# Kernel tuning notes

Measured on AMD Instinct MI355X. Metric: run time of the kernel, lower is better.

The kernel has to match this reference:

```python
import jax, jax.numpy as jnp
import numpy as np

B, T, M, D, H, DH = 2, 2048, 2048, 384, 4, 96
NM, DF, R, NA = 8, 1536, 16, 4
S = 0.02  # weight init scale

PARAM_NAMES = ['cWq','cbq','cWk','cbk','cWv','cbv','cWo','cbo',
               'sWq','sbq','sWk','sbk','sWv','sbv','sWo','sbo',
               'gW','gb','f1W','f1b','f2W','f2b','adA','adB',
               'ln1g','ln1b','ln2g','ln2b','ln3g','ln3b']

def setup_inputs() -> dict:
    key = jax.random.key(0)
    ks = jax.random.split(key, 20)
    n = lambda k, sh, s=1.0: jax.random.normal(k, sh, dtype=jnp.float32) * s
    z = lambda sh: jnp.zeros(sh, dtype=jnp.float32)
    o = lambda sh: jnp.ones(sh, dtype=jnp.float32)
    return {
        'x': n(ks[0], (B, T, D)),
        'mem': n(ks[1], (B, M, D)),
        'motif_ctrl': n(ks[2], (B, NM)),
        'adapter_idx': 1,
        'cWq': n(ks[3], (D, D), S), 'cbq': z((D,)),
        'cWk': n(ks[4], (D, D), S), 'cbk': z((D,)),
        'cWv': n(ks[5], (D, D), S), 'cbv': z((D,)),
        'cWo': n(ks[6], (D, D), S), 'cbo': z((D,)),
        'sWq': n(ks[7], (D, D), S), 'sbq': z((D,)),
        'sWk': n(ks[8], (D, D), S), 'sbk': z((D,)),
        'sWv': n(ks[9], (D, D), S), 'sbv': z((D,)),
        'sWo': n(ks[10], (D, D), S), 'sbo': z((D,)),
        'gW': n(ks[11], (H, NM), S), 'gb': z((H,)),
        'f1W': n(ks[12], (DF, D), S), 'f1b': z((DF,)),
        'f2W': n(ks[13], (D, DF), S), 'f2b': z((D,)),
        'adA': n(ks[14], (NA, R, D), S),
        'adB': n(ks[15], (NA, D, R), S),
        'ln1g': o((D,)), 'ln1b': z((D,)),
        'ln2g': o((D,)), 'ln2b': z((D,)),
        'ln3g': o((D,)), 'ln3b': z((D,)),
    }

def _lin(x, W, b):
    return x @ W.T + b  # torch nn.Linear convention: W is [out, in]

def _layernorm(x, g, b):
    mu = x.mean(-1, keepdims=True)
    var = ((x - mu) ** 2).mean(-1, keepdims=True)
    return (x - mu) * jax.lax.rsqrt(var + 1e-5) * g + b

def _block(x, mem, motif_ctrl, adapter_idx, p):
    scale = 1.0 / np.sqrt(DH).astype(np.float32)
    # --- cross-attention over memory ---
    h = _layernorm(x, p['ln1g'], p['ln1b'])
    q = _lin(h, p['cWq'], p['cbq']).reshape(B, T, H, DH)
    k = _lin(mem, p['cWk'], p['cbk']).reshape(B, M, H, DH)
    v = _lin(mem, p['cWv'], p['cbv']).reshape(B, M, H, DH)
    A = jax.nn.softmax(jnp.einsum('bthd,bmhd->bhtm', q, k) * scale, axis=-1)
    z = jnp.einsum('bhtm,bmhd->bthd', A, v).reshape(B, T, D)
    x = x + _lin(z, p['cWo'], p['cbo'])
    # --- motif-gated self-attention (post-softmax per-head gate) ---
    h = _layernorm(x, p['ln2g'], p['ln2b'])
    gates = jax.nn.sigmoid(motif_ctrl @ p['gW'].T + p['gb'])  # [B, H]
    q = _lin(h, p['sWq'], p['sbq']).reshape(B, T, H, DH)
    k = _lin(h, p['sWk'], p['sbk']).reshape(B, T, H, DH)
    v = _lin(h, p['sWv'], p['sbv']).reshape(B, T, H, DH)
    A = jax.nn.softmax(jnp.einsum('bthd,bshd->bhts', q, k) * scale, axis=-1)
    A = A * gates[:, :, None, None]
    z = jnp.einsum('bhts,bshd->bthd', A, v).reshape(B, T, D)
    x = x + _lin(z, p['sWo'], p['sbo'])
    # --- LoRA-adapter FFN ---
    h = _layernorm(x, p['ln3g'], p['ln3b'])
    f = _lin(jax.nn.gelu(_lin(h, p['f1W'], p['f1b']), approximate=False), p['f2W'], p['f2b'])
    f = f + (h @ p['adA'][adapter_idx].T) @ p['adB'][adapter_idx].T
    return x + f

def reference(x, mem, motif_ctrl, adapter_idx,
              cWq, cbq, cWk, cbk, cWv, cbv, cWo, cbo,
              sWq, sbq, sWk, sbk, sWv, sbv, sWo, sbo,
              gW, gb, f1W, f1b, f2W, f2b, adA, adB,
              ln1g, ln1b, ln2g, ln2b, ln3g, ln3b):
    p = dict(zip(PARAM_NAMES, (cWq, cbq, cWk, cbk, cWv, cbv, cWo, cbo,
                               sWq, sbq, sWk, sbk, sWv, sbv, sWo, sbo,
                               gW, gb, f1W, f1b, f2W, f2b, adA, adB,
                               ln1g, ln1b, ln2g, ln2b, ln3g, ln3b)))
    return _block(x, mem, motif_ctrl, int(adapter_idx), p)
```

## Files before the change

kernel.cpp:

```cpp
#include <hip/hip_runtime.h>
#include <hip/hip_bf16.h>
#include <math.h>

#define B_   2
#define T_   2048
#define M_   2048
#define D_   384
#define H_   4
#define DH_  96
#define NM_  8
#define DF_  1536
#define R_   16
#define NR_  4096

typedef unsigned short u16;
typedef u16    u16x8  __attribute__((ext_vector_type(8)));
typedef u16    u16x4  __attribute__((ext_vector_type(4)));
typedef __bf16 bf16x8 __attribute__((ext_vector_type(8)));
typedef float  f32x4  __attribute__((ext_vector_type(4)));

union V8 { u16x8 u; bf16x8 b; };
__device__ __forceinline__ bf16x8 as_bf(u16x8 x) { V8 v; v.u = x; return v.b; }

__device__ __forceinline__ u16 f2bf(float f) {
    unsigned u = __float_as_uint(f);
    unsigned r = (u + 0x7fffu + ((u >> 16) & 1u)) >> 16;
    return (u16)r;
}

__device__ __forceinline__ void load16(const u16* g, u16* l) {
    __builtin_amdgcn_global_load_lds(
        (const __attribute__((address_space(1))) void*)g,
        (__attribute__((address_space(3))) void*)l, 16, 0, 0);
}

__global__ __launch_bounds__(256)
void setup_kernel(const float* cWq, const float* cWk, const float* cWv, const float* cWo,
                  const float* sWq, const float* sWk, const float* sWv, const float* sWo,
                  const float* f1W, const float* f2W, const float* adA, const float* adB,
                  const float* mem,
                  u16* Wq_c, u16* Wkv_c, u16* Wco, u16* Wqkv_s, u16* Wso,
                  u16* Wf1, u16* Wf2, u16* WadA, u16* WadB, u16* memb,
                  const float* cbk, const float* cbv,
                  const float* sbq, const float* sbk, const float* sbv,
                  float* bkv_c, float* bqkv_s,
                  const float* mc, const float* gW, const float* gb, float* gates) {
    int seg = blockIdx.y;
    if (seg == 13) {
        for (int i = blockIdx.x * 256 + threadIdx.x; i < 1928; i += gridDim.x * 256) {
            if (i < 768) bkv_c[i] = (i < 384) ? cbk[i] : cbv[i - 384];
            else if (i < 1920) {
                int j = i - 768;
                bqkv_s[j] = (j < 384) ? sbq[j] : (j < 768 ? sbk[j - 384] : sbv[j - 768]);
            } else {
                int k = i - 1920;
                int b = k / H_, h = k % H_;
                float s = gb[h];
                for (int n = 0; n < NM_; n++)
                    s += mc[b * NM_ + n] * gW[h * NM_ + n];
                gates[k] = 1.f / (1.f + __expf(-s));
            }
        }
        return;
    }
    const float* s; u16* d; int n;
    switch (seg) {
        case 0:  s = cWq; d = Wq_c;            n = 147456; break;
        case 1:  s = cWk; d = Wkv_c;           n = 147456; break;
        case 2:  s = cWv; d = Wkv_c + 147456;  n = 147456; break;
        case 3:  s = cWo; d = Wco;             n = 147456; break;
        case 4:  s = sWq; d = Wqkv_s;          n = 147456; break;
        case 5:  s = sWk; d = Wqkv_s + 147456; n = 147456; break;
        case 6:  s = sWv; d = Wqkv_s + 294912; n = 147456; break;
        case 7:  s = sWo; d = Wso;             n = 147456; break;
        case 8:  s = f1W; d = Wf1;             n = 589824; break;
        case 9:  s = f2W; d = Wf2;             n = 589824; break;
        case 10: s = adA; d = WadA;            n = 24576;  break;
        case 11: s = adB; d = WadB;            n = 24576;  break;
        default: s = mem; d = memb;            n = 1572864; break;
    }
    for (int i = blockIdx.x * 256 + threadIdx.x; i < n; i += gridDim.x * 256)
        d[i] = f2bf(s[i]);
}

__global__ __launch_bounds__(384)
void ln_kernel(const float* __restrict__ x, const float* __restrict__ g,
               const float* __restrict__ b, u16* __restrict__ out) {
    __shared__ float sm[8];
    int row = blockIdx.x;
    int t = threadIdx.x;
    float v = x[(long)row * D_ + t];

    float s = v;
    for (int o = 32; o > 0; o >>= 1) s += __shfl_down(s, o);
    if ((t & 63) == 0) sm[t >> 6] = s;
    __syncthreads();
    float mu = 0.f;
    for (int i = 0; i < 6; i++) mu += sm[i];
    mu *= (1.f / D_);
    __syncthreads();

    float d = v - mu;
    s = d * d;
    for (int o = 32; o > 0; o >>= 1) s += __shfl_down(s, o);
    if ((t & 63) == 0) sm[t >> 6] = s;
    __syncthreads();
    float var = 0.f;
    for (int i = 0; i < 6; i++) var += sm[i];
    var *= (1.f / D_);

    float r = rsqrtf(var + 1e-5f);
    out[(long)row * D_ + t] = f2bf(d * r * g[t] + b[t]);
}

template<int ACT, bool OBF>
__global__ __launch_bounds__(256)
void gemm64(const u16* __restrict__ A, const u16* __restrict__ W,
            const float* __restrict__ bias, const float* __restrict__ res,
            void* __restrict__ Cout, int NC, int K) {
    __shared__ __align__(16) u16 As[4096];
    __shared__ __align__(16) u16 Ws[4096];
    int tid = threadIdx.x, w = tid >> 6, lane = tid & 63;
    int l15 = lane & 15, quad = lane >> 4;
    int bm = blockIdx.y * 64, bn = blockIdx.x * 64;
    int mt0 = (w & 1) * 2, nt0 = (w >> 1) * 2;

    const u16* Ag[2]; const u16* Wg[2]; u16* Al[2]; u16* Wl[2];
    #pragma unroll
    for (int i = 0; i < 2; i++) {
        int r = i * 4 + w, mt = r >> 1, kc = r & 1;
        Ag[i] = A + (long)(bm + mt * 16 + l15) * K + kc * 32 + quad * 8;
        Wg[i] = W + (long)(bn + mt * 16 + l15) * K + kc * 32 + quad * 8;
        Al[i] = As + r * 512;
        Wl[i] = Ws + r * 512;
    }

    f32x4 acc[2][2];
    #pragma unroll
    for (int i = 0; i < 2; i++)
        #pragma unroll
        for (int j = 0; j < 2; j++) acc[i][j] = (f32x4){0.f, 0.f, 0.f, 0.f};

    for (int k0 = 0; k0 < K; k0 += 64) {
        __syncthreads();
        #pragma unroll
        for (int i = 0; i < 2; i++) {
            load16(Ag[i] + k0, Al[i]);
            load16(Wg[i] + k0, Wl[i]);
        }
        __syncthreads();
        #pragma unroll
        for (int kc = 0; kc < 2; kc++) {
            u16x8 af[2], bfv[2];
            #pragma unroll
            for (int i = 0; i < 2; i++) {
                af[i]  = *(const u16x8*)(As + ((mt0 + i) * 2 + kc) * 512 + lane * 8);
                bfv[i] = *(const u16x8*)(Ws + ((nt0 + i) * 2 + kc) * 512 + lane * 8);
            }
            #pragma unroll
            for (int i = 0; i < 2; i++)
                #pragma unroll
                for (int j = 0; j < 2; j++)
                    acc[i][j] = __builtin_amdgcn_mfma_f32_16x16x32_bf16(
                        as_bf(af[i]), as_bf(bfv[j]), acc[i][j], 0, 0, 0);
        }
    }

    #pragma unroll
    for (int mi = 0; mi < 2; mi++) {
        #pragma unroll
        for (int nj = 0; nj < 2; nj++) {
            int col = bn + (nt0 + nj) * 16 + l15;
            float bv = bias ? bias[col] : 0.f;
            int rowb = bm + (mt0 + mi) * 16 + quad * 4;
            #pragma unroll
            for (int r = 0; r < 4; r++) {
                float v = acc[mi][nj][r] + bv;
                if (ACT == 1) v = 0.5f * v * (1.f + erff(v * 0.70710678118654752f));
                long idx = (long)(rowb + r) * NC + col;
                if (res) v += res[idx];
                if (OBF) ((u16*)Cout)[idx] = f2bf(v);
                else     ((float*)Cout)[idx] = v;
            }
        }
    }
}

template<int ACT, bool OBF>
__global__ __launch_bounds__(256)
void gemm_small(const u16* __restrict__ A, const u16* __restrict__ W,
                const float* __restrict__ bias, const float* __restrict__ res,
                void* __restrict__ Cout, int NR, int NC, int K,
                const int* __restrict__ aidx, int astride) {
    if (aidx) W += (long)aidx[0] * astride;
    __shared__ __align__(16) u16 As[2048];
    __shared__ __align__(16) u16 Ws[2048];
    int tid = threadIdx.x;
    int w = tid >> 6, lane = tid & 63;
    int bm = blockIdx.y * 64, bn = blockIdx.x * 64;
    int mt0 = (w & 1) * 2, nt0 = (w >> 1) * 2;

    int srow = ((tid >> 6) << 4) + (tid & 15);
    int kq8  = ((tid >> 4) & 3) * 8;
    const u16* Ag = A + (long)(bm + srow) * K + kq8;
    int wrow = bn + srow;
    const u16* Wg = W + (long)wrow * K + kq8;
    bool wok = wrow < NC;

    f32x4 acc[2][2];
    #pragma unroll
    for (int i = 0; i < 2; i++)
        #pragma unroll
        for (int j = 0; j < 2; j++) acc[i][j] = (f32x4){0.f, 0.f, 0.f, 0.f};

    for (int k0 = 0; k0 < K; k0 += 32) {
        u16x8 av = {0, 0, 0, 0, 0, 0, 0, 0};
        u16x8 wv = {0, 0, 0, 0, 0, 0, 0, 0};
        bool kok = (k0 + kq8) < K;
        if (kok) av = *(const u16x8*)(Ag + k0);
        if (kok && wok) wv = *(const u16x8*)(Wg + k0);
        __syncthreads();
        *(u16x8*)(As + tid * 8) = av;
        *(u16x8*)(Ws + tid * 8) = wv;
        __syncthreads();
        u16x8 af[2], bfv[2];
        #pragma unroll
        for (int i = 0; i < 2; i++) {
            af[i]  = *(const u16x8*)(As + (mt0 + i) * 512 + lane * 8);
            bfv[i] = *(const u16x8*)(Ws + (nt0 + i) * 512 + lane * 8);
        }
        #pragma unroll
        for (int i = 0; i < 2; i++)
            #pragma unroll
            for (int j = 0; j < 2; j++)
                acc[i][j] = __builtin_amdgcn_mfma_f32_16x16x32_bf16(
                    as_bf(af[i]), as_bf(bfv[j]), acc[i][j], 0, 0, 0);
    }

    int quad = lane >> 4, l15 = lane & 15;
    #pragma unroll
    for (int mi = 0; mi < 2; mi++) {
        #pragma unroll
        for (int nj = 0; nj < 2; nj++) {
            int col = bn + (nt0 + nj) * 16 + l15;
            if (col < NC) {
                float bv = bias ? bias[col] : 0.f;
                int rowb = bm + (mt0 + mi) * 16 + quad * 4;
                #pragma unroll
                for (int r = 0; r < 4; r++) {
                    float v = acc[mi][nj][r] + bv;
                    if (ACT == 1) v = 0.5f * v * (1.f + erff(v * 0.70710678118654752f));
                    long idx = (long)(rowb + r) * NC + col;
                    if (res) v += res[idx];
                    if (OBF) ((u16*)Cout)[idx] = f2bf(v);
                    else     ((float*)Cout)[idx] = v;
                }
            }
        }
    }
}

__global__ __launch_bounds__(256)
void transp_kernel(const u16* __restrict__ in, int istride, u16* __restrict__ out) {
    __shared__ __align__(16) u16 tile[64 * 72];
    int b = blockIdx.z;
    int r0 = blockIdx.x * 64;
    int c0 = blockIdx.y * 64;
    const u16* ib = in + (long)(b * 2048 + r0) * istride + c0;
    #pragma unroll
    for (int it = 0; it < 2; it++) {
        int c = threadIdx.x + it * 256;
        int i = c >> 3, jq = c & 7;
        *(u16x8*)&tile[i * 72 + jq * 8] = *(const u16x8*)(ib + (long)i * istride + jq * 8);
    }
    __syncthreads();
    u16* ob = out + (long)(b * 384 + c0) * 2048 + r0;
    #pragma unroll
    for (int it = 0; it < 2; it++) {
        int c = threadIdx.x + it * 256;
        int i2 = c >> 3, jq = c & 7;
        u16x8 v;
        #pragma unroll
        for (int e = 0; e < 8; e++) v[e] = tile[(jq * 8 + e) * 72 + i2];
        *(u16x8*)(ob + (long)i2 * 2048 + jq * 8) = v;
    }
}

__global__ __launch_bounds__(256)
void attn_mfma(const u16* __restrict__ Qg, int qs,
               const u16* __restrict__ Kg, int ks,
               const u16* __restrict__ Vt,
               float* __restrict__ Po, float* __restrict__ Pl) {
    __shared__ __align__(16) u16 Ks[6144];
    __shared__ __align__(16) u16 Vs[6144];
    __shared__ __align__(16) u16 Ps[4 * 1088];
    const float SCALE = 0.10206207261596575f;

    int tid = threadIdx.x, wv = tid >> 6, lane = tid & 63;
    int l15 = lane & 15, quad = lane >> 4;
    int bh = blockIdx.y, b = bh >> 2, h = bh & 3;
    int split = blockIdx.z;
    int q0 = blockIdx.x * 64 + wv * 16;

    const u16* Qb = Qg + (long)(b * 2048 + q0) * qs + h * 96;
    const u16* Kb = Kg + (long)(b * 2048 + split * 512) * ks + h * 96;
    const u16* Vb = Vt + (long)(b * 384 + h * 96) * 2048 + split * 512;

    u16x8 qf[3];
    #pragma unroll
    for (int t = 0; t < 3; t++)
        qf[t] = *(const u16x8*)(Qb + (long)l15 * qs + t * 32 + quad * 8);

    f32x4 o[6];
    #pragma unroll
    for (int i = 0; i < 6; i++) o[i] = (f32x4){0.f, 0.f, 0.f, 0.f};
    float rs[4] = {0.f, 0.f, 0.f, 0.f};
    u16* Pw = Ps + wv * 1088;

    const u16* KgI[3]; u16* KlI[3]; const u16* VgI[3]; u16* VlI[3];
    #pragma unroll
    for (int i = 0; i < 3; i++) {
        int r = i * 4 + wv;
        int ksub = r & 3, kst = r >> 2;
        KgI[i] = Kb + (long)(ksub * 16 + l15) * ks + kst * 32 + quad * 8;
        KlI[i] = Ks + (ksub * 3 + kst) * 512;
        int nt = r >> 1, t2 = r & 1;
        VgI[i] = Vb + (long)(nt * 16 + l15) * 2048 + t2 * 32 + quad * 8;
        VlI[i] = Vs + r * 512;
    }

    for (int j0 = 0; j0 < 512; j0 += 64) {
        __syncthreads();
        #pragma unroll
        for (int i = 0; i < 3; i++) {
            load16(KgI[i] + (long)j0 * ks, KlI[i]);
            load16(VgI[i] + j0, VlI[i]);
        }
        __syncthreads();

        f32x4 sc[4];
        #pragma unroll
        for (int s = 0; s < 4; s++) sc[s] = (f32x4){0.f, 0.f, 0.f, 0.f};
        #pragma unroll
        for (int s = 0; s < 4; s++)
            #pragma unroll
            for (int t = 0; t < 3; t++) {
                u16x8 kf = *(const u16x8*)(Ks + (s * 3 + t) * 512 + lane * 8);
                sc[s] = __builtin_amdgcn_mfma_f32_16x16x32_bf16(as_bf(qf[t]), as_bf(kf), sc[s], 0, 0, 0);
            }

        #pragma unroll
        for (int s = 0; s < 4; s++) {
            int base = (s >> 1) * 544 + ((((s & 1) << 1) | (l15 >> 3))) * 136 + (l15 & 7);
            #pragma unroll
            for (int r = 0; r < 4; r++) {
                float p = __expf(sc[s][r] * SCALE);
                rs[r] += p;
                Pw[base + (quad * 4 + r) * 8] = f2bf(p);
            }
        }
        #pragma unroll
        for (int t2 = 0; t2 < 2; t2++) {
            u16x8 pf = *(const u16x8*)(Pw + t2 * 544 + quad * 136 + l15 * 8);
            #pragma unroll
            for (int nt = 0; nt < 6; nt++) {
                u16x8 vf = *(const u16x8*)(Vs + (nt * 2 + t2) * 512 + lane * 8);
                o[nt] = __builtin_amdgcn_mfma_f32_16x16x32_bf16(as_bf(pf), as_bf(vf), o[nt], 0, 0, 0);
            }
        }
    }

    #pragma unroll
    for (int off = 1; off < 16; off <<= 1)
        #pragma unroll
        for (int r = 0; r < 4; r++) rs[r] += __shfl_xor(rs[r], off);

    float* Pob = Po + ((long)(split * 8 + bh) * 2048 + q0) * 96;
    #pragma unroll
    for (int nt = 0; nt < 6; nt++)
        #pragma unroll
        for (int r = 0; r < 4; r++)
            Pob[(long)(quad * 4 + r) * 96 + nt * 16 + l15] = o[nt][r];
    if (l15 == 0) {
        long mb = (long)(split * 8 + bh) * 2048 + q0 + quad * 4;
        #pragma unroll
        for (int r = 0; r < 4; r++) Pl[mb + r] = rs[r];
    }
}

__global__ __launch_bounds__(256)
void attn_combine(const float* __restrict__ Po, const float* __restrict__ Pl,
                  const float* __restrict__ gates, u16* __restrict__ Z) {
    int bh = blockIdx.y, b = bh >> 2, h = bh & 3;
    int tid = threadIdx.x;
    int rl = tid >> 2, part = tid & 3;
    int row = blockIdx.x * 64 + rl;
    long rbase = (long)bh * 2048 + row;

    float L = 0.f;
    #pragma unroll
    for (int s = 0; s < 4; s++) L += Pl[s * 16384 + rbase];
    float g = gates ? gates[bh] : 1.f;
    float sc = g / L;

    u16* Zr = Z + ((long)(b * 2048) + row) * 384 + h * 96 + part * 24;
    #pragma unroll
    for (int i = 0; i < 24; i += 4) {
        f32x4 acc = (f32x4){0.f, 0.f, 0.f, 0.f};
        #pragma unroll
        for (int s = 0; s < 4; s++) {
            f32x4 v = *(const f32x4*)(Po + ((long)s * 16384 + rbase) * 96 + part * 24 + i);
            #pragma unroll
            for (int e = 0; e < 4; e++) acc[e] += v[e];
        }
        u16x4 ov;
        #pragma unroll
        for (int e = 0; e < 4; e++) ov[e] = f2bf(acc[e] * sc);
        *(u16x4*)(Zr + i) = ov;
    }
}

extern "C" void kernel_launch(void* const* d_in, const int* in_sizes, int n_in,
                              void* d_out, int out_size, void* d_ws, size_t ws_size,
                              hipStream_t stream) {
    const float* x    = (const float*)d_in[0];
    const float* mem  = (const float*)d_in[1];
    const float* mc   = (const float*)d_in[2];
    const int*   aidx = (const int*)d_in[3];
    const float* cWq = (const float*)d_in[4],  *cbq = (const float*)d_in[5];
    const float* cWk = (const float*)d_in[6],  *cbk = (const float*)d_in[7];
    const float* cWv = (const float*)d_in[8],  *cbv = (const float*)d_in[9];
    const float* cWo = (const float*)d_in[10], *cbo = (const float*)d_in[11];
    const float* sWq = (const float*)d_in[12], *sbq = (const float*)d_in[13];
    const float* sWk = (const float*)d_in[14], *sbk = (const float*)d_in[15];
    const float* sWv = (const float*)d_in[16], *sbv = (const float*)d_in[17];
    const float* sWo = (const float*)d_in[18], *sbo = (const float*)d_in[19];
    const float* gW  = (const float*)d_in[20], *gb  = (const float*)d_in[21];
    const float* f1W = (const float*)d_in[22], *f1b = (const float*)d_in[23];
    const float* f2W = (const float*)d_in[24], *f2b = (const float*)d_in[25];
    const float* adA = (const float*)d_in[26], *adB = (const float*)d_in[27];
    const float* ln1g = (const float*)d_in[28], *ln1b = (const float*)d_in[29];
    const float* ln2g = (const float*)d_in[30], *ln2b = (const float*)d_in[31];
    const float* ln3g = (const float*)d_in[32], *ln3b = (const float*)d_in[33];

    u16* p = (u16*)d_ws;
    u16* H      = p; p += (size_t)NR_ * 384;
    u16* bufQ   = p; p += (size_t)NR_ * 384;
    u16* bufKV  = p; p += (size_t)NR_ * 768;
    u16* bufQKV = p; p += (size_t)NR_ * 1152;
    u16* Vt     = p; p += (size_t)B_ * 384 * 2048;
    u16* Zb     = p; p += (size_t)NR_ * 384;
    u16* F      = p; p += (size_t)NR_ * 1536;
    u16* Tl     = p; p += (size_t)NR_ * 16;
    u16* memb   = p; p += (size_t)NR_ * 384;
    u16* Wq_c   = p; p += 147456;
    u16* Wkv_c  = p; p += 294912;
    u16* Wco    = p; p += 147456;
    u16* Wqkv_s = p; p += 442368;
    u16* Wso    = p; p += 147456;
    u16* Wf1    = p; p += 589824;
    u16* Wf2    = p; p += 589824;
    u16* WadA   = p; p += 24576;
    u16* WadB   = p; p += 24576;
    float* fp = (float*)p;
    float* X1 = fp;     fp += (size_t)NR_ * 384;
    float* X2 = fp;     fp += (size_t)NR_ * 384;
    float* X3 = fp;     fp += (size_t)NR_ * 384;
    float* Po = fp;     fp += (size_t)4 * 8 * 2048 * 96;
    float* Pl = fp;     fp += (size_t)4 * 8 * 2048;
    float* bkv_c  = fp; fp += 768;
    float* bqkv_s = fp; fp += 1152;
    float* gbuf   = fp; fp += 8;

    setup_kernel<<<dim3(96, 14), 256, 0, stream>>>(
        cWq, cWk, cWv, cWo, sWq, sWk, sWv, sWo, f1W, f2W, adA, adB, mem,
        Wq_c, Wkv_c, Wco, Wqkv_s, Wso, Wf1, Wf2, WadA, WadB, memb,
        cbk, cbv, sbq, sbk, sbv, bkv_c, bqkv_s, mc, gW, gb, gbuf);

    const float* nf = nullptr;
    ln_kernel<<<NR_, 384, 0, stream>>>(x, ln1g, ln1b, H);
    gemm64<0, true><<<dim3(6, 64), 256, 0, stream>>>(H, Wq_c, cbq, nf, bufQ, 384, 384);
    gemm64<0, true><<<dim3(12, 64), 256, 0, stream>>>(memb, Wkv_c, bkv_c, nf, bufKV, 768, 384);
    transp_kernel<<<dim3(32, 6, 2), 256, 0, stream>>>(bufKV + 384, 768, Vt);
    attn_mfma<<<dim3(32, 8, 4), 256, 0, stream>>>(bufQ, 384, bufKV, 768, Vt, Po, Pl);
    attn_combine<<<dim3(32, 8), 256, 0, stream>>>(Po, Pl, nullptr, Zb);
    gemm64<0, false><<<dim3(6, 64), 256, 0, stream>>>(Zb, Wco, cbo, x, X1, 384, 384);

    ln_kernel<<<NR_, 384, 0, stream>>>(X1, ln2g, ln2b, H);
    gemm64<0, true><<<dim3(18, 64), 256, 0, stream>>>(H, Wqkv_s, bqkv_s, nf, bufQKV, 1152, 384);
    transp_kernel<<<dim3(32, 6, 2), 256, 0, stream>>>(bufQKV + 768, 1152, Vt);
    attn_mfma<<<dim3(32, 8, 4), 256, 0, stream>>>(bufQKV, 1152, bufQKV + 384, 1152, Vt, Po, Pl);
    attn_combine<<<dim3(32, 8), 256, 0, stream>>>(Po, Pl, gbuf, Zb);
    gemm64<0, false><<<dim3(6, 64), 256, 0, stream>>>(Zb, Wso, sbo, X1, X2, 384, 384);

    ln_kernel<<<NR_, 384, 0, stream>>>(X2, ln3g, ln3b, H);
    gemm64<1, true><<<dim3(24, 64), 256, 0, stream>>>(H, Wf1, f1b, nf, F, 1536, 384);
    gemm_small<0, true><<<dim3(1, 64), 256, 0, stream>>>(H, WadA, nullptr, nf, Tl, NR_, 16, 384, aidx, R_ * D_);
    gemm64<0, false><<<dim3(6, 64), 256, 0, stream>>>(F, Wf2, f2b, X2, X3, 384, 1536);
    gemm_small<0, false><<<dim3(6, 64), 256, 0, stream>>>(Tl, WadB, nullptr, X3, d_out, NR_, 384, 16, aidx, D_ * R_);
}
```

Measured before the change: 389.4 us.

## Double-buffer GEMM tiles and fuse V transpose and LoRA-B into GEMM epilogues

```diff
diff --git a/kernel.cpp b/kernel.cpp
--- a/kernel.cpp
+++ b/kernel.cpp
@@ -113,13 +113,16 @@
     out[(long)row * D_ + t] = f2bf(d * r * g[t] + b[t]);
 }
 
-template<int ACT, bool OBF>
+template<int ACT, bool OBF, bool VT, bool LORA>
 __global__ __launch_bounds__(256)
-void gemm64(const u16* __restrict__ A, const u16* __restrict__ W,
-            const float* __restrict__ bias, const float* __restrict__ res,
-            void* __restrict__ Cout, int NC, int K) {
-    __shared__ __align__(16) u16 As[4096];
-    __shared__ __align__(16) u16 Ws[4096];
+void gemm_pipe(const u16* __restrict__ A, const u16* __restrict__ W,
+               const float* __restrict__ bias, const float* __restrict__ res,
+               void* __restrict__ Cout, int NC, int K,
+               u16* __restrict__ Vt, int vtbase,
+               const u16* __restrict__ Tl, const u16* __restrict__ adB,
+               const int* __restrict__ aidx) {
+    __shared__ __align__(16) u16 As[8192];
+    __shared__ __align__(16) u16 Ws[8192];
     int tid = threadIdx.x, w = tid >> 6, lane = tid & 63;
     int l15 = lane & 15, quad = lane >> 4;
     int bm = blockIdx.y * 64, bn = blockIdx.x * 64;
@@ -127,12 +130,12 @@
 
     const u16* Ag[2]; const u16* Wg[2]; u16* Al[2]; u16* Wl[2];
     #pragma unroll
-    for (int i = 0; i < 2; i++) {
-        int r = i * 4 + w, mt = r >> 1, kc = r & 1;
-        Ag[i] = A + (long)(bm + mt * 16 + l15) * K + kc * 32 + quad * 8;
-        Wg[i] = W + (long)(bn + mt * 16 + l15) * K + kc * 32 + quad * 8;
-        Al[i] = As + r * 512;
-        Wl[i] = Ws + r * 512;
+    for (int s = 0; s < 2; s++) {
+        int r = s * 4 + w, mt = r >> 1, kc = r & 1;
+        Ag[s] = A + (long)(bm + mt * 16 + l15) * K + kc * 32 + quad * 8;
+        Wg[s] = W + (long)(bn + mt * 16 + l15) * K + kc * 32 + quad * 8;
+        Al[s] = As + r * 512;
+        Wl[s] = Ws + r * 512;
     }
 
     f32x4 acc[2][2];
@@ -141,29 +144,55 @@
         #pragma unroll
         for (int j = 0; j < 2; j++) acc[i][j] = (f32x4){0.f, 0.f, 0.f, 0.f};
 
-    for (int k0 = 0; k0 < K; k0 += 64) {
+    int niter = K >> 6;
+    #pragma unroll
+    for (int s = 0; s < 2; s++) { load16(Ag[s], Al[s]); load16(Wg[s], Wl[s]); }
+
+    for (int i = 0; i < niter; i++) {
         __syncthreads();
-        #pragma unroll
-        for (int i = 0; i < 2; i++) {
-            load16(Ag[i] + k0, Al[i]);
-            load16(Wg[i] + k0, Wl[i]);
-        }
-        __syncthreads();
+        int cur = (i & 1) * 4096, nxt = 4096 - cur;
+        if (i + 1 < niter) {
+            int k = (i + 1) << 6;
+            #pragma unroll
+            for (int s = 0; s < 2; s++) {
+                load16(Ag[s] + k, Al[s] + nxt);
+                load16(Wg[s] + k, Wl[s] + nxt);
+            }
+        }
         #pragma unroll
         for (int kc = 0; kc < 2; kc++) {
             u16x8 af[2], bfv[2];
             #pragma unroll
-            for (int i = 0; i < 2; i++) {
-                af[i]  = *(const u16x8*)(As + ((mt0 + i) * 2 + kc) * 512 + lane * 8);
-                bfv[i] = *(const u16x8*)(Ws + ((nt0 + i) * 2 + kc) * 512 + lane * 8);
-            }
-            #pragma unroll
-            for (int i = 0; i < 2; i++)
+            for (int s = 0; s < 2; s++) {
+                af[s]  = *(const u16x8*)(As + cur + ((mt0 + s) * 2 + kc) * 512 + lane * 8);
+                bfv[s] = *(const u16x8*)(Ws + cur + ((nt0 + s) * 2 + kc) * 512 + lane * 8);
+            }
+            #pragma unroll
+            for (int s = 0; s < 2; s++)
                 #pragma unroll
                 for (int j = 0; j < 2; j++)
-                    acc[i][j] = __builtin_amdgcn_mfma_f32_16x16x32_bf16(
-                        as_bf(af[i]), as_bf(bfv[j]), acc[i][j], 0, 0, 0);
-        }
+                    acc[s][j] = __builtin_amdgcn_mfma_f32_16x16x32_bf16(
+                        as_bf(af[s]), as_bf(bfv[j]), acc[s][j], 0, 0, 0);
+        }
+    }
+
+    if (LORA) {
+        long aoff = (long)aidx[0] * 6144;
+        u16x8 tlf[2] = {{0,0,0,0,0,0,0,0}, {0,0,0,0,0,0,0,0}};
+        u16x8 adf[2] = {{0,0,0,0,0,0,0,0}, {0,0,0,0,0,0,0,0}};
+        #pragma unroll
+        for (int s = 0; s < 2; s++) {
+            if (quad < 2) {
+                tlf[s] = *(const u16x8*)(Tl + (long)(bm + (mt0 + s) * 16 + l15) * 16 + quad * 8);
+                adf[s] = *(const u16x8*)(adB + aoff + (long)(bn + (nt0 + s) * 16 + l15) * 16 + quad * 8);
+            }
+        }
+        #pragma unroll
+        for (int s = 0; s < 2; s++)
+            #pragma unroll
+            for (int j = 0; j < 2; j++)
+                acc[s][j] = __builtin_amdgcn_mfma_f32_16x16x32_bf16(
+                    as_bf(tlf[s]), as_bf(adf[j]), acc[s][j], 0, 0, 0);
     }
 
     #pragma unroll
@@ -173,14 +202,23 @@
             int col = bn + (nt0 + nj) * 16 + l15;
             float bv = bias ? bias[col] : 0.f;
             int rowb = bm + (mt0 + mi) * 16 + quad * 4;
-            #pragma unroll
-            for (int r = 0; r < 4; r++) {
-                float v = acc[mi][nj][r] + bv;
-                if (ACT == 1) v = 0.5f * v * (1.f + erff(v * 0.70710678118654752f));
-                long idx = (long)(rowb + r) * NC + col;
-                if (res) v += res[idx];
-                if (OBF) ((u16*)Cout)[idx] = f2bf(v);
-                else     ((float*)Cout)[idx] = v;
+            if (VT && col >= vtbase) {
+                int vc = col - vtbase;
+                int b = rowb >> 11, rowl = rowb & 2047;
+                u16x4 ov;
+                #pragma unroll
+                for (int r = 0; r < 4; r++) ov[r] = f2bf(acc[mi][nj][r] + bv);
+                *(u16x4*)(Vt + ((long)b * 384 + vc) * 2048 + rowl) = ov;
+            } else {
+                #pragma unroll
+                for (int r = 0; r < 4; r++) {
+                    float v = acc[mi][nj][r] + bv;
+                    if (ACT == 1) v = 0.5f * v * (1.f + erff(v * 0.70710678118654752f));
+                    long idx = (long)(rowb + r) * NC + col;
+                    if (res) v += res[idx];
+                    if (OBF) ((u16*)Cout)[idx] = f2bf(v);
+                    else     ((float*)Cout)[idx] = v;
+                }
             }
         }
     }
@@ -257,32 +295,6 @@
                 }
             }
         }
-    }
-}
-
-__global__ __launch_bounds__(256)
-void transp_kernel(const u16* __restrict__ in, int istride, u16* __restrict__ out) {
-    __shared__ __align__(16) u16 tile[64 * 72];
-    int b = blockIdx.z;
-    int r0 = blockIdx.x * 64;
-    int c0 = blockIdx.y * 64;
-    const u16* ib = in + (long)(b * 2048 + r0) * istride + c0;
-    #pragma unroll
-    for (int it = 0; it < 2; it++) {
-        int c = threadIdx.x + it * 256;
-        int i = c >> 3, jq = c & 7;
-        *(u16x8*)&tile[i * 72 + jq * 8] = *(const u16x8*)(ib + (long)i * istride + jq * 8);
-    }
-    __syncthreads();
-    u16* ob = out + (long)(b * 384 + c0) * 2048 + r0;
-    #pragma unroll
-    for (int it = 0; it < 2; it++) {
-        int c = threadIdx.x + it * 256;
-        int i2 = c >> 3, jq = c & 7;
-        u16x8 v;
-        #pragma unroll
-        for (int e = 0; e < 8; e++) v[e] = tile[(jq * 8 + e) * 72 + i2];
-        *(u16x8*)(ob + (long)i2 * 2048 + jq * 8) = v;
     }
 }
 
@@ -465,7 +477,6 @@
     float* fp = (float*)p;
     float* X1 = fp;     fp += (size_t)NR_ * 384;
     float* X2 = fp;     fp += (size_t)NR_ * 384;
-    float* X3 = fp;     fp += (size_t)NR_ * 384;
     float* Po = fp;     fp += (size_t)4 * 8 * 2048 * 96;
     float* Pl = fp;     fp += (size_t)4 * 8 * 2048;
     float* bkv_c  = fp; fp += 768;
@@ -478,24 +489,22 @@
         cbk, cbv, sbq, sbk, sbv, bkv_c, bqkv_s, mc, gW, gb, gbuf);
 
     const float* nf = nullptr;
+    const u16* nu = nullptr;
     ln_kernel<<<NR_, 384, 0, stream>>>(x, ln1g, ln1b, H);
-    gemm64<0, true><<<dim3(6, 64), 256, 0, stream>>>(H, Wq_c, cbq, nf, bufQ, 384, 384);
-    gemm64<0, true><<<dim3(12, 64), 256, 0, stream>>>(memb, Wkv_c, bkv_c, nf, bufKV, 768, 384);
-    transp_kernel<<<dim3(32, 6, 2), 256, 0, stream>>>(bufKV + 384, 768, Vt);
+    gemm_pipe<0, true, false, false><<<dim3(6, 64), 256, 0, stream>>>(H, Wq_c, cbq, nf, bufQ, 384, 384, nullptr, 0, nu, nu, nullptr);
+    gemm_pipe<0, true, true, false><<<dim3(12, 64), 256, 0, stream>>>(memb, Wkv_c, bkv_c, nf, bufKV, 768, 384, Vt, 384, nu, nu, nullptr);
     attn_mfma<<<dim3(32, 8, 4), 256, 0, stream>>>(bufQ, 384, bufKV, 768, Vt, Po, Pl);
     attn_combine<<<dim3(32, 8), 256, 0, stream>>>(Po, Pl, nullptr, Zb);
-    gemm64<0, false><<<dim3(6, 64), 256, 0, stream>>>(Zb, Wco, cbo, x, X1, 384, 384);
+    gemm_pipe<0, false, false, false><<<dim3(6, 64), 256, 0, stream>>>(Zb, Wco, cbo, x, X1, 384, 384, nullptr, 0, nu, nu, nullptr);
 
     ln_kernel<<<NR_, 384, 0, stream>>>(X1, ln2g, ln2b, H);
-    gemm64<0, true><<<dim3(18, 64), 256, 0, stream>>>(H, Wqkv_s, bqkv_s, nf, bufQKV, 1152, 384);
-    transp_kernel<<<dim3(32, 6, 2), 256, 0, stream>>>(bufQKV + 768, 1152, Vt);
+    gemm_pipe<0, true, true, false><<<dim3(18, 64), 256, 0, stream>>>(H, Wqkv_s, bqkv_s, nf, bufQKV, 1152, 384, Vt, 768, nu, nu, nullptr);
     attn_mfma<<<dim3(32, 8, 4), 256, 0, stream>>>(bufQKV, 1152, bufQKV + 384, 1152, Vt, Po, Pl);
     attn_combine<<<dim3(32, 8), 256, 0, stream>>>(Po, Pl, gbuf, Zb);
-    gemm64<0, false><<<dim3(6, 64), 256, 0, stream>>>(Zb, Wso, sbo, X1, X2, 384, 384);
+    gemm_pipe<0, false, false, false><<<dim3(6, 64), 256, 0, stream>>>(Zb, Wso, sbo, X1, X2, 384, 384, nullptr, 0, nu, nu, nullptr);
 
     ln_kernel<<<NR_, 384, 0, stream>>>(X2, ln3g, ln3b, H);
-    gemm64<1, true><<<dim3(24, 64), 256, 0, stream>>>(H, Wf1, f1b, nf, F, 1536, 384);
+    gemm_pipe<1, true, false, false><<<dim3(24, 64), 256, 0, stream>>>(H, Wf1, f1b, nf, F, 1536, 384, nullptr, 0, nu, nu, nullptr);
     gemm_small<0, true><<<dim3(1, 64), 256, 0, stream>>>(H, WadA, nullptr, nf, Tl, NR_, 16, 384, aidx, R_ * D_);
-    gemm64<0, false><<<dim3(6, 64), 256, 0, stream>>>(F, Wf2, f2b, X2, X3, 384, 1536);
-    gemm_small<0, false><<<dim3(6, 64), 256, 0, stream>>>(Tl, WadB, nullptr, X3, d_out, NR_, 384, 16, aidx, D_ * R_);
-}
+    gemm_pipe<0, false, false, true><<<dim3(6, 64), 256, 0, stream>>>(F, Wf2, f2b, X2, d_out, 384, 1536, nullptr, 0, Tl, WadB, aidx);
+}
```

Measured after the change: 380.7 us. 2.2% less time.
